# Kernel optimization log

Measured on AMD Instinct MI355X. Metric: run time of the kernel, lower is better.

The kernel has to match this reference:

```python
import jax, jax.numpy as jnp
import numpy as np
from jax.ops import segment_sum

N_NODES = 100000
N_EDGES = 3200000
N_GRAPHS = 64


def gcn_conv(x, src, dst, W, b, num_nodes):
    h = x @ W  # [N, H]
    loop = jnp.arange(num_nodes, dtype=src.dtype)
    s = jnp.concatenate([src, loop])
    d = jnp.concatenate([dst, loop])
    deg = segment_sum(jnp.ones_like(d, dtype=h.dtype), d, num_segments=num_nodes)
    dinv = jnp.where(deg > 0, jax.lax.rsqrt(deg), 0.0)
    norm = dinv[s] * dinv[d]  # [E+N]
    msgs = h[s] * norm[:, None]  # gather + scale
    out = segment_sum(msgs, d, num_segments=num_nodes)  # scatter-add to targets
    return out + b


def setup_inputs() -> dict:
    key = jax.random.key(0)
    ks = jax.random.split(key, 8)
    F_IN, H, C = 128, 256, 2
    x = jax.random.normal(ks[0], (N_NODES, F_IN), dtype=jnp.float32)
    edge_index = jax.random.randint(ks[1], (2, N_EDGES), 0, N_NODES, dtype=jnp.int64)
    batch = jnp.sort(jax.random.randint(ks[2], (N_NODES,), 0, N_GRAPHS, dtype=jnp.int64))
    W1 = jax.random.normal(ks[3], (F_IN, H), dtype=jnp.float32) / np.sqrt(F_IN)
    b1 = jnp.zeros((H,), dtype=jnp.float32)
    W2 = jax.random.normal(ks[4], (H, H), dtype=jnp.float32) / np.sqrt(H)
    b2 = jnp.zeros((H,), dtype=jnp.float32)
    fc_w = jax.random.normal(ks[5], (H, C), dtype=jnp.float32) / np.sqrt(H)
    fc_b = jnp.zeros((C,), dtype=jnp.float32)
    return {"x": x, "edge_index": edge_index, "batch": batch, "W1": W1, "b1": b1,
            "W2": W2, "b2": b2, "fc_w": fc_w, "fc_b": fc_b}


def reference(x, edge_index, batch, W1, b1, W2, b2, fc_w, fc_b):
    src, dst = edge_index[0], edge_index[1]
    n = x.shape[0]
    h = jax.nn.relu(gcn_conv(x, src, dst, W1, b1, n))
    h = jax.nn.relu(gcn_conv(h, src, dst, W2, b2, n))
    # global_mean_pool over graph ids
    sums = segment_sum(h, batch, num_segments=N_GRAPHS)  # [G, H]
    cnts = segment_sum(jnp.ones((n,), dtype=h.dtype), batch, num_segments=N_GRAPHS)
    pooled = sums / jnp.maximum(cnts, 1.0)[:, None]
    logits = pooled @ fc_w + fc_b
    return jax.nn.log_softmax(logits, axis=1)
```

## Files before the change

### kernel.cpp

```cpp
#include <hip/hip_runtime.h>
#include <cstdint>

#define N_NODES 100000
#define N_EDGES 3200000
#define N_GRAPHS 64
#define HDIM 256
#define F_IN 128

#define BUCKET_BITS 7
#define NPB 128
#define N_BUCKETS ((N_NODES + NPB - 1) / NPB)
#define CHUNK 8192
#define NCHUNK ((N_EDGES + CHUNK - 1) / CHUNK)

typedef __attribute__((ext_vector_type(8))) short bf16x8;
typedef __attribute__((ext_vector_type(4))) float f32x4;
typedef __attribute__((ext_vector_type(2))) float f32x2;

__device__ __forceinline__ unsigned short f2bf(float f) {
    unsigned int b = __float_as_uint(f);
    b = (b + 0x7FFFu + ((b >> 16) & 1u)) >> 16;
    return (unsigned short)b;
}

__device__ __forceinline__ unsigned int pack4_fp8(float a, float b, float c, float d) {
    int v = 0;
    v = __builtin_amdgcn_cvt_pk_fp8_f32(a, b, v, false);
    v = __builtin_amdgcn_cvt_pk_fp8_f32(c, d, v, true);
    return (unsigned int)v;
}
__device__ __forceinline__ unsigned char pack1_fp8(float a) {
    int v = __builtin_amdgcn_cvt_pk_fp8_f32(a, a, 0, false);
    return (unsigned char)(v & 0xFF);
}

__global__ void zero_f(float* p, int n) {
    int i = blockIdx.x * blockDim.x + threadIdx.x;
    if (i < n) p[i] = 0.0f;
}

__global__ __launch_bounds__(256) void block_count(const int* __restrict__ dst,
                                                   int* __restrict__ counts, int nE) {
    __shared__ int hist[N_BUCKETS];
    int blk = blockIdx.x, t = threadIdx.x;
    for (int i = t; i < N_BUCKETS; i += 256) hist[i] = 0;
    __syncthreads();
    int lo = blk * CHUNK;
    int hi = lo + CHUNK < nE ? lo + CHUNK : nE;
    for (int i = lo + t; i < hi; i += 256) atomicAdd(&hist[dst[i] >> BUCKET_BITS], 1);
    __syncthreads();
    for (int i = t; i < N_BUCKETS; i += 256) counts[blk * N_BUCKETS + i] = hist[i];
}

__global__ __launch_bounds__(256) void bucket_totals(const int* __restrict__ counts,
                                                     int* __restrict__ tot) {
    __shared__ int red[256];
    int b = blockIdx.x, t = threadIdx.x;
    int s = 0;
    for (int blk = t; blk < NCHUNK; blk += 256) s += counts[blk * N_BUCKETS + b];
    red[t] = s;
    __syncthreads();
    for (int o = 128; o > 0; o >>= 1) {
        if (t < o) red[t] += red[t + o];
        __syncthreads();
    }
    if (t == 0) tot[b] = red[0];
}

__global__ __launch_bounds__(1024) void scan_buckets(const int* __restrict__ tot,
                                                     int* __restrict__ base, int nb) {
    __shared__ int lds[1024];
    int t = threadIdx.x;
    int v = (t < nb) ? tot[t] : 0;
    lds[t] = v;
    __syncthreads();
    for (int off = 1; off < 1024; off <<= 1) {
        int a = (t >= off) ? lds[t - off] : 0;
        __syncthreads();
        lds[t] += a;
        __syncthreads();
    }
    int excl = lds[t] - v;
    if (t < nb) base[t] = excl;
    if (t == nb) base[t] = excl;
}

__global__ __launch_bounds__(512) void column_scan(const int* __restrict__ counts,
                                                   const int* __restrict__ base,
                                                   int* __restrict__ offs) {
    __shared__ int lds[512];
    int b = blockIdx.x, t = threadIdx.x;
    int v = (t < NCHUNK) ? counts[t * N_BUCKETS + b] : 0;
    lds[t] = v;
    __syncthreads();
    for (int off = 1; off < 512; off <<= 1) {
        int a = (t >= off) ? lds[t - off] : 0;
        __syncthreads();
        lds[t] += a;
        __syncthreads();
    }
    if (t < NCHUNK) offs[t * N_BUCKETS + b] = base[b] + lds[t] - v;
}

__global__ __launch_bounds__(256) void block_scatter(const int* __restrict__ src,
                                                     const int* __restrict__ dst,
                                                     const int* __restrict__ offs,
                                                     unsigned int* __restrict__ rec, int nE) {
    __shared__ int cur[N_BUCKETS];
    int blk = blockIdx.x, t = threadIdx.x;
    for (int i = t; i < N_BUCKETS; i += 256) cur[i] = offs[blk * N_BUCKETS + i];
    __syncthreads();
    int lo = blk * CHUNK;
    int hi = lo + CHUNK < nE ? lo + CHUNK : nE;
    for (int i = lo + t; i < hi; i += 256) {
        int d = dst[i];
        int b = d >> BUCKET_BITS;
        int pos = atomicAdd(&cur[b], 1);
        rec[pos] = (unsigned int)src[i] | ((unsigned int)(d & (NPB - 1)) << 17);
    }
}

__global__ __launch_bounds__(512) void bucket_csr(const unsigned int* __restrict__ rec,
                                                  const int* __restrict__ base,
                                                  int* __restrict__ ptr, float* __restrict__ dinv,
                                                  int* __restrict__ csr_src, int n) {
    __shared__ int hist[NPB];
    __shared__ int sc[NPB];
    __shared__ int cur[NPB];
    int b = blockIdx.x;
    int lo = base[b], hi = base[b + 1];
    int t = threadIdx.x;
    if (t < NPB) hist[t] = 0;
    __syncthreads();
    for (int i = lo + t; i < hi; i += 512) atomicAdd(&hist[rec[i] >> 17], 1);
    __syncthreads();
    if (t < NPB) sc[t] = hist[t];
    __syncthreads();
    for (int off = 1; off < NPB; off <<= 1) {
        int a = (t < NPB && t >= off) ? sc[t - off] : 0;
        __syncthreads();
        if (t < NPB) sc[t] += a;
        __syncthreads();
    }
    if (t < NPB) {
        int node = b * NPB + t;
        int incl = sc[t];
        int excl = incl - hist[t];
        if (node < n) {
            ptr[node] = lo + incl;
            dinv[node] = rsqrtf((float)hist[t] + 1.0f);
        }
        cur[t] = lo + excl;
    }
    __syncthreads();
    for (int i = lo + t; i < hi; i += 512) {
        unsigned int r = rec[i];
        int pos = atomicAdd(&cur[r >> 17], 1);
        csr_src[pos] = (int)(r & 0x1FFFFu);
    }
}

__global__ void convert_x_pre(const float* __restrict__ x, const float* __restrict__ dinv,
                              unsigned int* __restrict__ xp, int n) {
    int tid = blockIdx.x * blockDim.x + threadIdx.x;
    if (tid >= n * (F_IN / 4)) return;
    int node = tid / (F_IN / 4);
    float di = dinv[node];
    float4 v = ((const float4*)x)[tid];
    xp[tid] = pack4_fp8(v.x * di, v.y * di, v.z * di, v.w * di);
}

__global__ void pack_w(const float* __restrict__ W, unsigned short* __restrict__ hi,
                       unsigned short* __restrict__ lo, int K) {
    int idx = blockIdx.x * blockDim.x + threadIdx.x;
    if (idx >= K * HDIM) return;
    int k = idx >> 8, c = idx & 255;
    float w = W[idx];
    unsigned short h = f2bf(w);
    float hf = __uint_as_float((unsigned int)h << 16);
    unsigned short l = f2bf(w - hf);
    int pos = ((k >> 5) * 16 + (c >> 4)) * 512 + ((((k >> 3) & 3) * 16) + (c & 15)) * 8 + (k & 7);
    hi[pos] = h;
    lo[pos] = l;
}

__global__ void csr_agg128_fp8(const unsigned char* __restrict__ h, const int* __restrict__ ptr,
                               const int* __restrict__ csr, const float* __restrict__ dinv,
                               unsigned short* __restrict__ out, int n) {
    int wave = threadIdx.x >> 6, lane = threadIdx.x & 63;
    int node = blockIdx.x * 4 + wave;
    if (node >= n) return;
    int begin = node ? ptr[node - 1] : 0;
    int end = ptr[node];
    unsigned int u = *(const unsigned short*)(h + (size_t)node * 128 + lane * 2);
    f32x2 a01 = __builtin_amdgcn_cvt_pk_f32_fp8((int)u, false);
    int i = begin;
    for (; i + 16 <= end; i += 16) {
        unsigned int uu[16];
#pragma unroll
        for (int j = 0; j < 16; j++) {
            int s = csr[i + j];
            uu[j] = *(const unsigned short*)(h + (size_t)s * 128 + lane * 2);
        }
#pragma unroll
        for (int j = 0; j < 16; j++)
            a01 += __builtin_amdgcn_cvt_pk_f32_fp8((int)uu[j], false);
    }
    for (; i + 4 <= end; i += 4) {
        unsigned int uu[4];
#pragma unroll
        for (int j = 0; j < 4; j++) {
            int s = csr[i + j];
            uu[j] = *(const unsigned short*)(h + (size_t)s * 128 + lane * 2);
        }
#pragma unroll
        for (int j = 0; j < 4; j++)
            a01 += __builtin_amdgcn_cvt_pk_f32_fp8((int)uu[j], false);
    }
    for (; i < end; i++) {
        int s = csr[i];
        unsigned int u0 = *(const unsigned short*)(h + (size_t)s * 128 + lane * 2);
        a01 += __builtin_amdgcn_cvt_pk_f32_fp8((int)u0, false);
    }
    float dn = dinv[node];
    unsigned int o = (unsigned int)f2bf(a01.x * dn) | ((unsigned int)f2bf(a01.y * dn) << 16);
    *(unsigned int*)(out + (size_t)node * 128 + lane * 2) = o;
}

__global__ void csr_agg256_fp8(const unsigned char* __restrict__ h, const int* __restrict__ ptr,
                               const int* __restrict__ csr, const float* __restrict__ dinv,
                               unsigned short* __restrict__ out, int n) {
    int wave = threadIdx.x >> 6, lane = threadIdx.x & 63;
    int node = blockIdx.x * 4 + wave;
    if (node >= n) return;
    int begin = node ? ptr[node - 1] : 0;
    int end = ptr[node];
    unsigned int u = *(const unsigned int*)(h + (size_t)node * 256 + lane * 4);
    f32x2 a01 = __builtin_amdgcn_cvt_pk_f32_fp8((int)u, false);
    f32x2 a23 = __builtin_amdgcn_cvt_pk_f32_fp8((int)u, true);
    int i = begin;
    for (; i + 16 <= end; i += 16) {
        unsigned int uu[16];
#pragma unroll
        for (int j = 0; j < 16; j++) {
            int s = csr[i + j];
            uu[j] = *(const unsigned int*)(h + (size_t)s * 256 + lane * 4);
        }
#pragma unroll
        for (int j = 0; j < 16; j++) {
            a01 += __builtin_amdgcn_cvt_pk_f32_fp8((int)uu[j], false);
            a23 += __builtin_amdgcn_cvt_pk_f32_fp8((int)uu[j], true);
        }
    }
    for (; i + 4 <= end; i += 4) {
        unsigned int uu[4];
#pragma unroll
        for (int j = 0; j < 4; j++) {
            int s = csr[i + j];
            uu[j] = *(const unsigned int*)(h + (size_t)s * 256 + lane * 4);
        }
#pragma unroll
        for (int j = 0; j < 4; j++) {
            a01 += __builtin_amdgcn_cvt_pk_f32_fp8((int)uu[j], false);
            a23 += __builtin_amdgcn_cvt_pk_f32_fp8((int)uu[j], true);
        }
    }
    for (; i < end; i++) {
        int s = csr[i];
        unsigned int u0 = *(const unsigned int*)(h + (size_t)s * 256 + lane * 4);
        a01 += __builtin_amdgcn_cvt_pk_f32_fp8((int)u0, false);
        a23 += __builtin_amdgcn_cvt_pk_f32_fp8((int)u0, true);
    }
    float dn = dinv[node];
    uint2 o;
    o.x = (unsigned int)f2bf(a01.x * dn) | ((unsigned int)f2bf(a01.y * dn) << 16);
    o.y = (unsigned int)f2bf(a23.x * dn) | ((unsigned int)f2bf(a23.y * dn) << 16);
    *(uint2*)(out + (size_t)node * 256 + lane * 4) = o;
}

template <int K, int MODE>
__global__ __launch_bounds__(256, 3) void gemm_mfma(
    const unsigned short* __restrict__ A, const unsigned short* __restrict__ Whi,
    const unsigned short* __restrict__ Wlo, const float* __restrict__ bias,
    const float* __restrict__ dinv, const int* __restrict__ batch,
    float* __restrict__ pool, void* __restrict__ outp, int n) {
    __shared__ float lpool[4 * 256];
    int wave = threadIdx.x >> 6, lane = threadIdx.x & 63;
    int quad = lane >> 4, l16 = lane & 15;
    int rowgrp = wave >> 1, colhalf = wave & 1;
    int blockrow = blockIdx.x * 64;
    int rowbase = blockrow + rowgrp * 32;

    if (MODE == 1) {
        for (int i = threadIdx.x; i < 4 * 256; i += 256) lpool[i] = 0.0f;
        __syncthreads();
    }

    f32x4 acc[2][8];
#pragma unroll
    for (int s = 0; s < 2; s++)
#pragma unroll
        for (int ct = 0; ct < 8; ct++) acc[s][ct] = (f32x4){0.f, 0.f, 0.f, 0.f};

    int r0 = rowbase + l16;
    int r1 = rowbase + 16 + l16;
    int rc0 = r0 < n ? r0 : n - 1;
    int rc1 = r1 < n ? r1 : n - 1;

    for (int kt = 0; kt < K / 32; kt++) {
        bf16x8 a0 = *(const bf16x8*)(A + (size_t)rc0 * K + kt * 32 + quad * 8);
        bf16x8 a1 = *(const bf16x8*)(A + (size_t)rc1 * K + kt * 32 + quad * 8);
        const unsigned short* wh = Whi + ((size_t)kt * 16 + colhalf * 8) * 512 + lane * 8;
        const unsigned short* wl = Wlo + ((size_t)kt * 16 + colhalf * 8) * 512 + lane * 8;
#pragma unroll
        for (int ct = 0; ct < 8; ct++) {
            bf16x8 bh = *(const bf16x8*)(wh + ct * 512);
            bf16x8 bl = *(const bf16x8*)(wl + ct * 512);
            acc[0][ct] = __builtin_amdgcn_mfma_f32_16x16x32_bf16(a0, bh, acc[0][ct], 0, 0, 0);
            acc[0][ct] = __builtin_amdgcn_mfma_f32_16x16x32_bf16(a0, bl, acc[0][ct], 0, 0, 0);
            acc[1][ct] = __builtin_amdgcn_mfma_f32_16x16x32_bf16(a1, bh, acc[1][ct], 0, 0, 0);
            acc[1][ct] = __builtin_amdgcn_mfma_f32_16x16x32_bf16(a1, bl, acc[1][ct], 0, 0, 0);
        }
    }

    if (MODE == 0) {
#pragma unroll
        for (int s = 0; s < 2; s++) {
#pragma unroll
            for (int ct = 0; ct < 8; ct++) {
                int col = colhalf * 128 + ct * 16 + l16;
                float b = bias[col];
#pragma unroll
                for (int r = 0; r < 4; r++) {
                    int row = rowbase + s * 16 + quad * 4 + r;
                    if (row < n) {
                        float v = acc[s][ct][r] + b;
                        v = v > 0.0f ? v : 0.0f;
                        ((unsigned char*)outp)[(size_t)row * HDIM + col] = pack1_fp8(v * dinv[row]);
                    }
                }
            }
        }
    } else {
        int g0 = batch[blockrow < n ? blockrow : n - 1];
        int gr[2][4];
#pragma unroll
        for (int s = 0; s < 2; s++)
#pragma unroll
            for (int r = 0; r < 4; r++) {
                int row = rowbase + s * 16 + quad * 4 + r;
                gr[s][r] = (row < n) ? batch[row] : -1;
            }
#pragma unroll
        for (int s = 0; s < 2; s++) {
#pragma unroll
            for (int ct = 0; ct < 8; ct++) {
                int col = colhalf * 128 + ct * 16 + l16;
                float b = bias[col];
#pragma unroll
                for (int r = 0; r < 4; r++) {
                    int g = gr[s][r];
                    if (g >= 0) {
                        float v = acc[s][ct][r] + b;
                        v = v > 0.0f ? v : 0.0f;
                        int slot = g - g0;
                        if (slot < 4) {
                            atomicAdd(&lpool[slot * 256 + col], v);
                        } else {
                            atomicAdd(&pool[g * HDIM + col], v);
                        }
                    }
                }
            }
        }
        __syncthreads();
        for (int i = threadIdx.x; i < 4 * 256; i += 256) {
            float val = lpool[i];
            if (val != 0.0f) {
                int slot = i >> 8, col = i & 255;
                atomicAdd(&pool[(g0 + slot) * HDIM + col], val);
            }
        }
    }
}

__global__ void final_head(const float* __restrict__ pool, const int* __restrict__ batch,
                           const float* __restrict__ fcw, const float* __restrict__ fcb,
                           float* __restrict__ out, int n) {
    int g = threadIdx.x;
    if (g < N_GRAPHS) {
        int lo = 0, hi = n;
        while (lo < hi) { int m = (lo + hi) >> 1; if (batch[m] < g) lo = m + 1; else hi = m; }
        int b0 = lo;
        lo = 0; hi = n;
        while (lo < hi) { int m = (lo + hi) >> 1; if (batch[m] < g + 1) lo = m + 1; else hi = m; }
        int c = lo - b0;
        float cf = c > 1 ? (float)c : 1.0f;
        float inv = 1.0f / cf;
        float l0 = fcb[0], l1 = fcb[1];
        for (int f = 0; f < HDIM; f++) {
            float p = pool[g * HDIM + f] * inv;
            l0 += p * fcw[f * 2 + 0];
            l1 += p * fcw[f * 2 + 1];
        }
        float m = fmaxf(l0, l1);
        float lse = m + logf(expf(l0 - m) + expf(l1 - m));
        out[g * 2 + 0] = l0 - lse;
        out[g * 2 + 1] = l1 - lse;
    }
}

extern "C" void kernel_launch(void* const* d_in, const int* in_sizes, int n_in,
                              void* d_out, int out_size, void* d_ws, size_t ws_size,
                              hipStream_t stream) {
    const float* x = (const float*)d_in[0];
    const int* ei = (const int*)d_in[1];
    const int* batch = (const int*)d_in[2];
    const float* W1 = (const float*)d_in[3];
    const float* b1 = (const float*)d_in[4];
    const float* W2 = (const float*)d_in[5];
    const float* b2 = (const float*)d_in[6];
    const float* fcw = (const float*)d_in[7];
    const float* fcb = (const float*)d_in[8];
    float* out = (float*)d_out;

    const int* src = ei;
    const int* dst = ei + N_EDGES;

    char* ws = (char*)d_ws;
    float* dinv = (float*)ws;            ws += 4 * ((N_NODES + 255) & ~255);
    int* ptr = (int*)ws;                 ws += 4 * ((N_NODES + 255) & ~255);
    int* csr_src = (int*)ws;             ws += 4 * (size_t)N_EDGES;
    int* counts = (int*)ws;              ws += 4 * (size_t)NCHUNK * N_BUCKETS;
    int* offs = (int*)ws;                ws += 4 * (size_t)NCHUNK * N_BUCKETS;
    int* tot = (int*)ws;                 ws += 4 * 1024;
    int* bbase = (int*)ws;               ws += 4 * 1024;
    unsigned short* W1hi = (unsigned short*)ws; ws += 2 * F_IN * HDIM;
    unsigned short* W1lo = (unsigned short*)ws; ws += 2 * F_IN * HDIM;
    unsigned short* W2hi = (unsigned short*)ws; ws += 2 * HDIM * HDIM;
    unsigned short* W2lo = (unsigned short*)ws; ws += 2 * HDIM * HDIM;
    float* pool = (float*)ws;            ws += 4 * N_GRAPHS * HDIM;
    char* R0 = ws;                       ws += 4 * (size_t)N_NODES * HDIM;
    unsigned char* x_pre = (unsigned char*)R0;
    unsigned short* A1 = (unsigned short*)(R0 + (size_t)N_NODES * F_IN);
    unsigned char* h1_pre = (unsigned char*)(R0 + 3 * (size_t)N_NODES * F_IN);
    unsigned short* A2 = (unsigned short*)ws;
    unsigned int* records = (unsigned int*)A2;

    block_count<<<NCHUNK, 256, 0, stream>>>(dst, counts, N_EDGES);
    bucket_totals<<<N_BUCKETS, 256, 0, stream>>>(counts, tot);
    scan_buckets<<<1, 1024, 0, stream>>>(tot, bbase, N_BUCKETS);
    column_scan<<<N_BUCKETS, 512, 0, stream>>>(counts, bbase, offs);
    block_scatter<<<NCHUNK, 256, 0, stream>>>(src, dst, offs, records, N_EDGES);
    bucket_csr<<<N_BUCKETS, 512, 0, stream>>>(records, bbase, ptr, dinv, csr_src, N_NODES);

    convert_x_pre<<<(N_NODES * (F_IN / 4) + 255) / 256, 256, 0, stream>>>(
        x, dinv, (unsigned int*)x_pre, N_NODES);
    pack_w<<<(F_IN * HDIM + 255) / 256, 256, 0, stream>>>(W1, W1hi, W1lo, F_IN);
    pack_w<<<(HDIM * HDIM + 255) / 256, 256, 0, stream>>>(W2, W2hi, W2lo, HDIM);
    zero_f<<<(N_GRAPHS * HDIM + 255) / 256, 256, 0, stream>>>(pool, N_GRAPHS * HDIM);

    csr_agg128_fp8<<<(N_NODES + 3) / 4, 256, 0, stream>>>(x_pre, ptr, csr_src, dinv, A1, N_NODES);
    gemm_mfma<F_IN, 0><<<(N_NODES + 63) / 64, 256, 0, stream>>>(A1, W1hi, W1lo, b1, dinv,
                                                                nullptr, nullptr, h1_pre, N_NODES);
    csr_agg256_fp8<<<(N_NODES + 3) / 4, 256, 0, stream>>>(h1_pre, ptr, csr_src, dinv, A2, N_NODES);
    gemm_mfma<HDIM, 1><<<(N_NODES + 63) / 64, 256, 0, stream>>>(A2, W2hi, W2lo, b2, dinv,
                                                                batch, pool, nullptr, N_NODES);

    final_head<<<1, 64, 0, stream>>>(pool, batch, fcw, fcb, out, N_NODES);
}
```

Measured before the change: 733.3 us.

## Unfuse mean-pool from layer-2 GEMM into separate run-length pooling kernel

The second GEMM no longer does per-element shared and global atomic adds into the pool. It now writes the ReLU output to a bf16 buffer. A new kernel sums contiguous runs of nodes per graph for each feature and issues one atomic per run. This drops the large atomic traffic from the GEMM epilogue, at the cost of writing and re-reading a 100000x256 bf16 tensor and rounding activations to bf16 before pooling.

```diff
diff --git a/kernel.cpp b/kernel.cpp
--- a/kernel.cpp
+++ b/kernel.cpp
@@ -21,6 +21,9 @@
     unsigned int b = __float_as_uint(f);
     b = (b + 0x7FFFu + ((b >> 16) & 1u)) >> 16;
     return (unsigned short)b;
+}
+__device__ __forceinline__ float bf2f(unsigned short u) {
+    return __uint_as_float((unsigned int)u << 16);
 }
 
 __device__ __forceinline__ unsigned int pack4_fp8(float a, float b, float c, float d) {
@@ -282,19 +285,11 @@
 __global__ __launch_bounds__(256, 3) void gemm_mfma(
     const unsigned short* __restrict__ A, const unsigned short* __restrict__ Whi,
     const unsigned short* __restrict__ Wlo, const float* __restrict__ bias,
-    const float* __restrict__ dinv, const int* __restrict__ batch,
-    float* __restrict__ pool, void* __restrict__ outp, int n) {
-    __shared__ float lpool[4 * 256];
+    const float* __restrict__ dinv, void* __restrict__ outp, int n) {
     int wave = threadIdx.x >> 6, lane = threadIdx.x & 63;
     int quad = lane >> 4, l16 = lane & 15;
     int rowgrp = wave >> 1, colhalf = wave & 1;
-    int blockrow = blockIdx.x * 64;
-    int rowbase = blockrow + rowgrp * 32;
-
-    if (MODE == 1) {
-        for (int i = threadIdx.x; i < 4 * 256; i += 256) lpool[i] = 0.0f;
-        __syncthreads();
-    }
+    int rowbase = blockIdx.x * 64 + rowgrp * 32;
 
     f32x4 acc[2][8];
 #pragma unroll
@@ -323,65 +318,47 @@
         }
     }
 
-    if (MODE == 0) {
-#pragma unroll
-        for (int s = 0; s < 2; s++) {
-#pragma unroll
-            for (int ct = 0; ct < 8; ct++) {
-                int col = colhalf * 128 + ct * 16 + l16;
-                float b = bias[col];
-#pragma unroll
-                for (int r = 0; r < 4; r++) {
-                    int row = rowbase + s * 16 + quad * 4 + r;
-                    if (row < n) {
-                        float v = acc[s][ct][r] + b;
-                        v = v > 0.0f ? v : 0.0f;
+#pragma unroll
+    for (int s = 0; s < 2; s++) {
+#pragma unroll
+        for (int ct = 0; ct < 8; ct++) {
+            int col = colhalf * 128 + ct * 16 + l16;
+            float b = bias[col];
+#pragma unroll
+            for (int r = 0; r < 4; r++) {
+                int row = rowbase + s * 16 + quad * 4 + r;
+                if (row < n) {
+                    float v = acc[s][ct][r] + b;
+                    v = v > 0.0f ? v : 0.0f;
+                    if (MODE == 0) {
                         ((unsigned char*)outp)[(size_t)row * HDIM + col] = pack1_fp8(v * dinv[row]);
+                    } else {
+                        ((unsigned short*)outp)[(size_t)row * HDIM + col] = f2bf(v);
                     }
                 }
             }
         }
-    } else {
-        int g0 = batch[blockrow < n ? blockrow : n - 1];
-        int gr[2][4];
-#pragma unroll
-        for (int s = 0; s < 2; s++)
-#pragma unroll
-            for (int r = 0; r < 4; r++) {
-                int row = rowbase + s * 16 + quad * 4 + r;
-                gr[s][r] = (row < n) ? batch[row] : -1;
-            }
-#pragma unroll
-        for (int s = 0; s < 2; s++) {
-#pragma unroll
-            for (int ct = 0; ct < 8; ct++) {
-                int col = colhalf * 128 + ct * 16 + l16;
-                float b = bias[col];
-#pragma unroll
-                for (int r = 0; r < 4; r++) {
-                    int g = gr[s][r];
-                    if (g >= 0) {
-                        float v = acc[s][ct][r] + b;
-                        v = v > 0.0f ? v : 0.0f;
-                        int slot = g - g0;
-                        if (slot < 4) {
-                            atomicAdd(&lpool[slot * 256 + col], v);
-                        } else {
-                            atomicAdd(&pool[g * HDIM + col], v);
-                        }
-                    }
-                }
-            }
-        }
-        __syncthreads();
-        for (int i = threadIdx.x; i < 4 * 256; i += 256) {
-            float val = lpool[i];
-            if (val != 0.0f) {
-                int slot = i >> 8, col = i & 255;
-                atomicAdd(&pool[(g0 + slot) * HDIM + col], val);
-            }
-        }
-    }
+    }
+}
+
+__global__ void pool_sum_runs(const unsigned short* __restrict__ h, const int* __restrict__ batch,
+                              float* __restrict__ pool, int n) {
+    constexpr int ROWS = 128;
+    int f = threadIdx.x;
+    int r0 = blockIdx.x * ROWS;
+    int rend = r0 + ROWS;
+    if (rend > n) rend = n;
+    float acc = 0.0f;
+    int cur = batch[r0];
+    for (int r = r0; r < rend; r++) {
+        int g = batch[r];
+        if (g != cur) {
+            atomicAdd(&pool[cur * HDIM + f], acc);
+            acc = 0.0f; cur = g;
+        }
+        acc += bf2f(h[(size_t)r * HDIM + f]);
+    }
+    atomicAdd(&pool[cur * HDIM + f], acc);
 }
 
 __global__ void final_head(const float* __restrict__ pool, const int* __restrict__ batch,
@@ -444,6 +421,7 @@
     unsigned char* x_pre = (unsigned char*)R0;
     unsigned short* A1 = (unsigned short*)(R0 + (size_t)N_NODES * F_IN);
     unsigned char* h1_pre = (unsigned char*)(R0 + 3 * (size_t)N_NODES * F_IN);
+    unsigned short* h2 = (unsigned short*)R0;
     unsigned short* A2 = (unsigned short*)ws;
     unsigned int* records = (unsigned int*)A2;
 
@@ -462,10 +440,11 @@
 
     csr_agg128_fp8<<<(N_NODES + 3) / 4, 256, 0, stream>>>(x_pre, ptr, csr_src, dinv, A1, N_NODES);
     gemm_mfma<F_IN, 0><<<(N_NODES + 63) / 64, 256, 0, stream>>>(A1, W1hi, W1lo, b1, dinv,
-                                                                nullptr, nullptr, h1_pre, N_NODES);
+                                                                h1_pre, N_NODES);
     csr_agg256_fp8<<<(N_NODES + 3) / 4, 256, 0, stream>>>(h1_pre, ptr, csr_src, dinv, A2, N_NODES);
-    gemm_mfma<HDIM, 1><<<(N_NODES + 63) / 64, 256, 0, stream>>>(A2, W2hi, W2lo, b2, dinv,
-                                                                batch, pool, nullptr, N_NODES);
-
+    gemm_mfma<HDIM, 2><<<(N_NODES + 63) / 64, 256, 0, stream>>>(A2, W2hi, W2lo, b2, dinv,
+                                                                h2, N_NODES);
+
+    pool_sum_runs<<<(N_NODES + 127) / 128, 256, 0, stream>>>(h2, batch, pool, N_NODES);
     final_head<<<1, 64, 0, stream>>>(pool, batch, fcw, fcb, out, N_NODES);
 }
```

Result: faster. 650.8 us (median of 2 runs) (-11.3%).
